# Kernel optimization log

Measured on AMD Instinct MI355X. Metric: run time of the kernel, lower is better.

## Reference

```python
import jax, jax.numpy as jnp
import numpy as np

N_NODES = 50000
N_EDGES = 800000
D_FEAT = 64
THETA = [0.5, 0.3, 0.15, 0.05]  # polynomial filter coefficients, k = len(THETA)


def setup_inputs() -> dict:
    key = jax.random.key(0)
    k1, k2, k3 = jax.random.split(key, 3)
    feat = jax.random.normal(k1, (N_NODES, D_FEAT), dtype=jnp.float32)
    src = jax.random.randint(k2, (N_EDGES,), 0, N_NODES)  # A[src, dst] = 1
    dst = jax.random.randint(k3, (N_EDGES,), 0, N_NODES)
    return {"feat": feat, "src": src, "dst": dst}


def reference(feat, src, dst):
    # normalize_adj: D^{-1/2} A^T D^{-1/2} with D = rowsum(A) (inf -> 0 for isolated nodes).
    n = feat.shape[0]
    deg = jax.ops.segment_sum(jnp.ones(src.shape, dtype=feat.dtype), src, num_segments=n)
    d_inv_sqrt = jnp.where(deg > 0, jax.lax.rsqrt(jnp.maximum(deg, 1.0)), jnp.zeros_like(deg))
    # norm[i, j] = d_i^{-1/2} A[j, i] d_j^{-1/2}; edge (src=j, dst=i) carries weight
    w = d_inv_sqrt[src] * d_inv_sqrt[dst]  # [E]

    def spmm(x):
        # (A_norm @ x)[i] = sum over edges with dst==i of w_e * x[src_e]
        return jax.ops.segment_sum(w[:, None] * x[src], dst, num_segments=n)

    # Original loop: h = theta[0]*(A@f); for k>=1: f = A@f; h += theta[k]*f.
    # Note theta[0] and theta[1] both scale A@f0 (feat is not updated before h init),
    # so we fold them together and avoid recomputing the first SpMM.
    x = spmm(feat)  # A @ f0, shared by the k=0 and k=1 terms
    h = (THETA[0] + THETA[1]) * x
    for k in range(2, len(THETA)):
        x = spmm(x)
        h = h + THETA[k] * x
    return h
```

## Files before the change

kernel.cpp:

```cpp
#include <hip/hip_runtime.h>
#include <hip/hip_bf16.h>

#define N_NODES 50000
#define N_EDGES 800000
#define D_FEAT  64
#define NW      12500
#define G_SRC   64
#define G_DST   256
#define CONV_NB 128
#define FILL_NB 64
#define HB      512
#define SCAN_B  256
#define SCAN_NBLK ((NW + SCAN_B - 1) / SCAN_B)
#define CAP     48


typedef unsigned uint4_ev  __attribute__((ext_vector_type(4)));
typedef float    float4_ev __attribute__((ext_vector_type(4)));

__device__ __forceinline__ float bflo(unsigned u) { return __uint_as_float(u << 16); }
__device__ __forceinline__ float bfhi(unsigned u) { return __uint_as_float(u & 0xFFFF0000u); }
__device__ __forceinline__ unsigned pack_bf16(float a, float b) {
    __hip_bfloat16 x = __float2bfloat16(a), y = __float2bfloat16(b);
    unsigned short ux = *reinterpret_cast<unsigned short*>(&x);
    unsigned short uy = *reinterpret_cast<unsigned short*>(&y);
    return (unsigned)ux | ((unsigned)uy << 16);
}


__global__ void hist_cv_kernel(const int* __restrict__ src, const int* __restrict__ dst,
                               unsigned* __restrict__ psrc_p, unsigned* __restrict__ pdst_p,
                               const float* __restrict__ feat, unsigned* __restrict__ featbf,
                               unsigned* __restrict__ csr, int nE) {
    int t = threadIdx.x;
    int b = blockIdx.x;
    if (b >= G_SRC + G_DST + CONV_NB) {
        int fb = b - (G_SRC + G_DST + CONV_NB);
        uint4* c4 = (uint4*)csr;
        const int n4 = N_NODES * CAP / 4;
        const int nthr = FILL_NB * HB;
        uint4 z = make_uint4(0u, 0u, 0u, 0u);
        for (int i = fb * HB + t; i < n4; i += nthr) c4[i] = z;
        return;
    }
    if (b >= G_SRC + G_DST) {
        int cb = b - (G_SRC + G_DST);
        const float4* f4 = (const float4*)feat;
        uint2* fb2 = (uint2*)featbf;
        const int nthr = CONV_NB * HB;
        for (int i = cb * HB + t; i < N_NODES * 16; i += nthr) {
            float4 v = f4[i];
            fb2[i] = make_uint2(pack_bf16(v.x, v.y), pack_bf16(v.z, v.w));
        }
        return;
    }
    __shared__ unsigned bins[NW];
    for (int i = t; i < NW; i += HB) bins[i] = 0;
    __syncthreads();
    bool is_src = (b < G_SRC);
    int g = is_src ? b : (b - G_SRC);
    int nstr = is_src ? G_SRC : G_DST;
    const int4* k4 = (const int4*)(is_src ? src : dst);
    int nE4 = nE >> 2;
    for (int q = g * HB + t; q < nE4; q += nstr * HB) {
        int4 kv = k4[q];
        atomicAdd(&bins[kv.x >> 2], 1u << (8 * (kv.x & 3)));
        atomicAdd(&bins[kv.y >> 2], 1u << (8 * (kv.y & 3)));
        atomicAdd(&bins[kv.z >> 2], 1u << (8 * (kv.z & 3)));
        atomicAdd(&bins[kv.w >> 2], 1u << (8 * (kv.w & 3)));
    }
    __syncthreads();
    unsigned* p = (is_src ? psrc_p : pdst_p) + g * NW;
    for (int i = t; i < NW; i += HB) p[i] = bins[i];
}

__global__ void scanA_kernel(const unsigned* __restrict__ pdst_p, const unsigned* __restrict__ psrc_p,
                             unsigned* __restrict__ gbase_p, unsigned* __restrict__ deg_p,
                             float* __restrict__ dinv) {
    int w = blockIdx.x * SCAN_B + threadIdx.x;
    if (w >= NW) return;
    unsigned td = 0;
    #pragma unroll 16
    for (int g = 0; g < G_DST; g++) {
        gbase_p[g * NW + w] = td;
        td += pdst_p[g * NW + w];
    }
    deg_p[w] = td;
    unsigned ts = 0;
    #pragma unroll 16
    for (int g = 0; g < G_SRC; g++) ts += psrc_p[g * NW + w];
    unsigned d0 = ts & 255u, d1 = (ts >> 8) & 255u, d2 = (ts >> 16) & 255u, d3 = ts >> 24;
    float4 dv;
    dv.x = d0 ? rsqrtf((float)d0) : 0.0f;
    dv.y = d1 ? rsqrtf((float)d1) : 0.0f;
    dv.z = d2 ? rsqrtf((float)d2) : 0.0f;
    dv.w = d3 ? rsqrtf((float)d3) : 0.0f;
    ((float4*)dinv)[w] = dv;
}

__global__ void scatter_kernel(const int* __restrict__ src, const int* __restrict__ dst,
                               const unsigned* __restrict__ gbase_p, const float* __restrict__ dinv,
                               unsigned* __restrict__ csr, int nE) {
    __shared__ unsigned cur[NW];
    int t = threadIdx.x;
    int g = blockIdx.x;
    const unsigned* gb = gbase_p + (size_t)g * NW;
    for (int i = t; i < NW; i += HB) cur[i] = gb[i];
    __syncthreads();
    const int4* s4 = (const int4*)src;
    const int4* d4 = (const int4*)dst;
    int nE4 = nE >> 2;
    for (int q = g * HB + t; q < nE4; q += G_DST * HB) {
        int4 sv = s4[q];
        int4 dv = d4[q];
        {
            int k = dv.x; int sh = 8 * (k & 3);
            unsigned old = atomicAdd(&cur[k >> 2], 1u << sh);
            unsigned pw = __float2uint_rn(dinv[sv.x] * 32767.0f);
            csr[(size_t)k * CAP + ((old >> sh) & 255u)] = (pw << 17) | (unsigned)sv.x;
        }
        {
            int k = dv.y; int sh = 8 * (k & 3);
            unsigned old = atomicAdd(&cur[k >> 2], 1u << sh);
            unsigned pw = __float2uint_rn(dinv[sv.y] * 32767.0f);
            csr[(size_t)k * CAP + ((old >> sh) & 255u)] = (pw << 17) | (unsigned)sv.y;
        }
        {
            int k = dv.z; int sh = 8 * (k & 3);
            unsigned old = atomicAdd(&cur[k >> 2], 1u << sh);
            unsigned pw = __float2uint_rn(dinv[sv.z] * 32767.0f);
            csr[(size_t)k * CAP + ((old >> sh) & 255u)] = (pw << 17) | (unsigned)sv.z;
        }
        {
            int k = dv.w; int sh = 8 * (k & 3);
            unsigned old = atomicAdd(&cur[k >> 2], 1u << sh);
            unsigned pw = __float2uint_rn(dinv[sv.w] * 32767.0f);
            csr[(size_t)k * CAP + ((old >> sh) & 255u)] = (pw << 17) | (unsigned)sv.w;
        }
    }
}


__device__ __forceinline__ unsigned get_deg(const unsigned* __restrict__ deg_p, int i) {
    return (deg_p[(unsigned)i >> 2] >> (8 * (i & 3))) & 255u;
}

struct Acc8 { float a0, a1, a2, a3, a4, a5, a6, a7; };

__device__ __forceinline__ Acc8 spmm_accum(int ii, int mdr, const unsigned* __restrict__ csr,
                                           const unsigned* __restrict__ x, int c8) {
    const unsigned* row = csr + (size_t)ii * CAP;
    const uint4* x4 = (const uint4*)x;
    const float WS = 1.0f / 32767.0f;
    float a0 = 0, a1 = 0, a2 = 0, a3 = 0, a4 = 0, a5 = 0, a6 = 0, a7 = 0;
    for (int s = 0; s < mdr; s += 4) {
        unsigned v0 = __builtin_nontemporal_load(row + s);
        unsigned v1 = __builtin_nontemporal_load(row + s + 1);
        unsigned v2 = __builtin_nontemporal_load(row + s + 2);
        unsigned v3 = __builtin_nontemporal_load(row + s + 3);
        int   s0 = (int)(v0 & 0x1FFFFu); float w0 = (float)(v0 >> 17) * WS;
        int   s1 = (int)(v1 & 0x1FFFFu); float w1 = (float)(v1 >> 17) * WS;
        int   s2 = (int)(v2 & 0x1FFFFu); float w2 = (float)(v2 >> 17) * WS;
        int   s3 = (int)(v3 & 0x1FFFFu); float w3 = (float)(v3 >> 17) * WS;
        uint4 r0 = x4[(size_t)s0 * 8 + c8];
        uint4 r1 = x4[(size_t)s1 * 8 + c8];
        uint4 r2 = x4[(size_t)s2 * 8 + c8];
        uint4 r3 = x4[(size_t)s3 * 8 + c8];
        a0 += w0 * bflo(r0.x) + w1 * bflo(r1.x) + w2 * bflo(r2.x) + w3 * bflo(r3.x);
        a1 += w0 * bfhi(r0.x) + w1 * bfhi(r1.x) + w2 * bfhi(r2.x) + w3 * bfhi(r3.x);
        a2 += w0 * bflo(r0.y) + w1 * bflo(r1.y) + w2 * bflo(r2.y) + w3 * bflo(r3.y);
        a3 += w0 * bfhi(r0.y) + w1 * bfhi(r1.y) + w2 * bfhi(r2.y) + w3 * bfhi(r3.y);
        a4 += w0 * bflo(r0.z) + w1 * bflo(r1.z) + w2 * bflo(r2.z) + w3 * bflo(r3.z);
        a5 += w0 * bfhi(r0.z) + w1 * bfhi(r1.z) + w2 * bfhi(r2.z) + w3 * bfhi(r3.z);
        a6 += w0 * bflo(r0.w) + w1 * bflo(r1.w) + w2 * bflo(r2.w) + w3 * bflo(r3.w);
        a7 += w0 * bfhi(r0.w) + w1 * bfhi(r1.w) + w2 * bfhi(r2.w) + w3 * bfhi(r3.w);
    }
    Acc8 r = {a0, a1, a2, a3, a4, a5, a6, a7};
    return r;
}

__global__ void spmm_mid_kernel(const unsigned* __restrict__ csr, const unsigned* __restrict__ deg_p,
                                const float* __restrict__ dinv,
                                const unsigned* __restrict__ x, unsigned* __restrict__ y) {
    int tid = blockIdx.x * blockDim.x + threadIdx.x;
    int lane = threadIdx.x & 63;
    int g = lane >> 3, c8 = lane & 7;
    int i = (tid >> 6) * 8 + g;
    bool valid = i < N_NODES;
    int ii = valid ? i : 0;
    int md = valid ? (int)get_deg(deg_p, ii) : 0;
    md = max(md, __shfl_xor(md, 8));
    md = max(md, __shfl_xor(md, 16));
    md = max(md, __shfl_xor(md, 32));
    int mdr = (md + 3) & ~3;
    Acc8 A = spmm_accum(ii, mdr, csr, x, c8);
    if (valid) {
        float di = dinv[i];
        uint4_ev p;
        p.x = pack_bf16(A.a0 * di, A.a1 * di);
        p.y = pack_bf16(A.a2 * di, A.a3 * di);
        p.z = pack_bf16(A.a4 * di, A.a5 * di);
        p.w = pack_bf16(A.a6 * di, A.a7 * di);
        __builtin_nontemporal_store(p, (uint4_ev*)y + (size_t)i * 8 + c8);
    }
}

__global__ void spmm_final_kernel(const unsigned* __restrict__ csr, const unsigned* __restrict__ deg_p,
                                  const float* __restrict__ dinv,
                                  const unsigned* __restrict__ x1, const unsigned* __restrict__ x2,
                                  float* __restrict__ h) {
    int tid = blockIdx.x * blockDim.x + threadIdx.x;
    int lane = threadIdx.x & 63;
    int g = lane >> 3, c8 = lane & 7;
    int i = (tid >> 6) * 8 + g;
    bool valid = i < N_NODES;
    int ii = valid ? i : 0;
    int md = valid ? (int)get_deg(deg_p, ii) : 0;
    md = max(md, __shfl_xor(md, 8));
    md = max(md, __shfl_xor(md, 16));
    md = max(md, __shfl_xor(md, 32));
    int mdr = (md + 3) & ~3;
    Acc8 A = spmm_accum(ii, mdr, csr, x2, c8);
    if (valid) {
        float di = dinv[i] * 0.05f;
        uint4 u1 = ((const uint4*)x1)[(size_t)i * 8 + c8];
        uint4 u2 = ((const uint4*)x2)[(size_t)i * 8 + c8];
        float4_ev o0, o1;
        o0.x = 0.8f * bflo(u1.x) + 0.15f * bflo(u2.x) + di * A.a0;
        o0.y = 0.8f * bfhi(u1.x) + 0.15f * bfhi(u2.x) + di * A.a1;
        o0.z = 0.8f * bflo(u1.y) + 0.15f * bflo(u2.y) + di * A.a2;
        o0.w = 0.8f * bfhi(u1.y) + 0.15f * bfhi(u2.y) + di * A.a3;
        o1.x = 0.8f * bflo(u1.z) + 0.15f * bflo(u2.z) + di * A.a4;
        o1.y = 0.8f * bfhi(u1.z) + 0.15f * bfhi(u2.z) + di * A.a5;
        o1.z = 0.8f * bflo(u1.w) + 0.15f * bflo(u2.w) + di * A.a6;
        o1.w = 0.8f * bfhi(u1.w) + 0.15f * bfhi(u2.w) + di * A.a7;
        float* hp = h + (size_t)i * 64 + c8 * 8;
        __builtin_nontemporal_store(o0, (float4_ev*)hp);
        __builtin_nontemporal_store(o1, (float4_ev*)(hp + 4));
    }
}


extern "C" void kernel_launch(void* const* d_in, const int* in_sizes, int n_in,
                              void* d_out, int out_size, void* d_ws, size_t ws_size,
                              hipStream_t stream) {
    const float* feat = (const float*)d_in[0];
    const int*   src  = (const int*)d_in[1];
    const int*   dst  = (const int*)d_in[2];
    float* h = (float*)d_out;

    char* ws = (char*)d_ws;
    unsigned* psrc_p   = (unsigned*)(ws);
    unsigned* pdst_p   = (unsigned*)(ws +  3200000u);
    unsigned* gbase_p  = (unsigned*)(ws + 16000000u);
    float*    dinv     = (float*)   (ws + 28800000u);
    unsigned* csr      = (unsigned*)(ws + 29000192u);
    unsigned* featbf   = (unsigned*)(ws + 38600192u);
    unsigned* bufA     = (unsigned*)(ws + 45000192u);
    unsigned* bufB     = (unsigned*)(ws + 51400192u);
    unsigned* deg_p    = (unsigned*)(ws + 57800192u);

    const int nE = N_EDGES;
    const int B = 256;

    hist_cv_kernel<<<G_SRC + G_DST + CONV_NB + FILL_NB, HB, 0, stream>>>(
        src, dst, psrc_p, pdst_p, feat, featbf, csr, nE);

    scanA_kernel<<<SCAN_NBLK, SCAN_B, 0, stream>>>(pdst_p, psrc_p, gbase_p, deg_p, dinv);

    scatter_kernel<<<G_DST, HB, 0, stream>>>(src, dst, gbase_p, dinv, csr, nE);

    const int spmmGrid = (N_NODES * 8 + B - 1) / B;
    spmm_mid_kernel<<<spmmGrid, B, 0, stream>>>(csr, deg_p, dinv, featbf, bufA);
    spmm_mid_kernel<<<spmmGrid, B, 0, stream>>>(csr, deg_p, dinv, bufA, bufB);
    spmm_final_kernel<<<spmmGrid, B, 0, stream>>>(csr, deg_p, dinv, bufA, bufB, h);
}
```

Measured before the change: 159.2 us.

## Fold degree normalization into features and shrink CSR to 16-bit indices

Rescales the propagated vectors by D^{-1/2} so the SpMM becomes an unweighted gather-sum. The per-edge weights can then be dropped, and CSR entries shrink from packed 32-bit index+weight to 16-bit indices. Padding slots point to a zero sentinel row, which removes the weight decode and multiply. Feature conversion now happens in the scatter kernel, scaled by dinv, and the final kernel rescales with sqrt(deg). Node indices must fit in 16 bits (50000 does), and storing the rescaled values in bf16 may change rounding error.

Result: faster. 150.2 us (-5.6%).

```diff
diff --git a/kernel.cpp b/kernel.cpp
--- a/kernel.cpp
+++ b/kernel.cpp
@@ -3,19 +3,17 @@
 
 #define N_NODES 50000
 #define N_EDGES 800000
-#define D_FEAT  64
 #define NW      12500
 #define G_SRC   64
 #define G_DST   256
-#define CONV_NB 128
-#define FILL_NB 64
+#define PRE_NB  64
 #define HB      512
-#define SCAN_B  256
-#define SCAN_NBLK ((NW + SCAN_B - 1) / SCAN_B)
+#define SCAN_B  512
+#define SCAN_NBLK 25
 #define CAP     48
-
-
-typedef unsigned uint4_ev  __attribute__((ext_vector_type(4)));
+#define ZROW    50000
+
+
 typedef float    float4_ev __attribute__((ext_vector_type(4)));
 
 __device__ __forceinline__ float bflo(unsigned u) { return __uint_as_float(u << 16); }
@@ -27,30 +25,28 @@
     return (unsigned)ux | ((unsigned)uy << 16);
 }
 
-
-__global__ void hist_cv_kernel(const int* __restrict__ src, const int* __restrict__ dst,
-                               unsigned* __restrict__ psrc_p, unsigned* __restrict__ pdst_p,
-                               const float* __restrict__ feat, unsigned* __restrict__ featbf,
-                               unsigned* __restrict__ csr, int nE) {
+__device__ __forceinline__ unsigned get_deg(const unsigned* __restrict__ deg_p, int i) {
+    return (deg_p[(unsigned)i >> 2] >> (8 * (i & 3))) & 255u;
+}
+
+__global__ void build1_kernel(const int* __restrict__ src, const int* __restrict__ dst,
+                              unsigned* __restrict__ psrc_p, unsigned* __restrict__ pdst_p,
+                              unsigned short* __restrict__ csr16,
+                              unsigned* __restrict__ z0, unsigned* __restrict__ z1,
+                              unsigned* __restrict__ z2, int nE) {
     int t = threadIdx.x;
     int b = blockIdx.x;
-    if (b >= G_SRC + G_DST + CONV_NB) {
-        int fb = b - (G_SRC + G_DST + CONV_NB);
-        uint4* c4 = (uint4*)csr;
-        const int n4 = N_NODES * CAP / 4;
-        const int nthr = FILL_NB * HB;
-        uint4 z = make_uint4(0u, 0u, 0u, 0u);
-        for (int i = fb * HB + t; i < n4; i += nthr) c4[i] = z;
-        return;
-    }
+    int nE4 = nE >> 2;
     if (b >= G_SRC + G_DST) {
-        int cb = b - (G_SRC + G_DST);
-        const float4* f4 = (const float4*)feat;
-        uint2* fb2 = (uint2*)featbf;
-        const int nthr = CONV_NB * HB;
-        for (int i = cb * HB + t; i < N_NODES * 16; i += nthr) {
-            float4 v = f4[i];
-            fb2[i] = make_uint2(pack_bf16(v.x, v.y), pack_bf16(v.z, v.w));
+        int fb = b - (G_SRC + G_DST);
+        uint4* c4 = (uint4*)csr16;
+        const int n4 = N_NODES * CAP / 8;
+        const unsigned SEN2 = ((unsigned)ZROW << 16) | (unsigned)ZROW;
+        uint4 zz = make_uint4(SEN2, SEN2, SEN2, SEN2);
+        for (int i = fb * HB + t; i < n4; i += PRE_NB * HB) c4[i] = zz;
+        if (fb == 0 && t < 96) {
+            unsigned* zp = (t < 32) ? z0 : (t < 64) ? z1 : z2;
+            zp[(size_t)ZROW * 32 + (t & 31)] = 0u;
         }
         return;
     }
@@ -61,7 +57,6 @@
     int g = is_src ? b : (b - G_SRC);
     int nstr = is_src ? G_SRC : G_DST;
     const int4* k4 = (const int4*)(is_src ? src : dst);
-    int nE4 = nE >> 2;
     for (int q = g * HB + t; q < nE4; q += nstr * HB) {
         int4 kv = k4[q];
         atomicAdd(&bins[kv.x >> 2], 1u << (8 * (kv.x & 3)));
@@ -70,170 +65,164 @@
         atomicAdd(&bins[kv.w >> 2], 1u << (8 * (kv.w & 3)));
     }
     __syncthreads();
-    unsigned* p = (is_src ? psrc_p : pdst_p) + g * NW;
+    unsigned* p = (is_src ? psrc_p : pdst_p) + (size_t)g * NW;
     for (int i = t; i < NW; i += HB) p[i] = bins[i];
 }
 
-__global__ void scanA_kernel(const unsigned* __restrict__ pdst_p, const unsigned* __restrict__ psrc_p,
-                             unsigned* __restrict__ gbase_p, unsigned* __restrict__ deg_p,
-                             float* __restrict__ dinv) {
+__global__ void scan_kernel(const unsigned* __restrict__ pdst_p, const unsigned* __restrict__ psrc_p,
+                            unsigned* __restrict__ gbase_p, unsigned* __restrict__ deg_p,
+                            float* __restrict__ dinv, float* __restrict__ sd) {
     int w = blockIdx.x * SCAN_B + threadIdx.x;
     if (w >= NW) return;
     unsigned td = 0;
     #pragma unroll 16
     for (int g = 0; g < G_DST; g++) {
-        gbase_p[g * NW + w] = td;
-        td += pdst_p[g * NW + w];
+        gbase_p[(size_t)g * NW + w] = td;
+        td += pdst_p[(size_t)g * NW + w];
     }
     deg_p[w] = td;
     unsigned ts = 0;
     #pragma unroll 16
-    for (int g = 0; g < G_SRC; g++) ts += psrc_p[g * NW + w];
+    for (int g = 0; g < G_SRC; g++) ts += psrc_p[(size_t)g * NW + w];
     unsigned d0 = ts & 255u, d1 = (ts >> 8) & 255u, d2 = (ts >> 16) & 255u, d3 = ts >> 24;
-    float4 dv;
-    dv.x = d0 ? rsqrtf((float)d0) : 0.0f;
-    dv.y = d1 ? rsqrtf((float)d1) : 0.0f;
-    dv.z = d2 ? rsqrtf((float)d2) : 0.0f;
-    dv.w = d3 ? rsqrtf((float)d3) : 0.0f;
+    float4 dv, sv;
+    dv.x = d0 ? rsqrtf((float)d0) : 0.0f;  sv.x = d0 ? sqrtf((float)d0) : 0.0f;
+    dv.y = d1 ? rsqrtf((float)d1) : 0.0f;  sv.y = d1 ? sqrtf((float)d1) : 0.0f;
+    dv.z = d2 ? rsqrtf((float)d2) : 0.0f;  sv.z = d2 ? sqrtf((float)d2) : 0.0f;
+    dv.w = d3 ? rsqrtf((float)d3) : 0.0f;  sv.w = d3 ? sqrtf((float)d3) : 0.0f;
     ((float4*)dinv)[w] = dv;
-}
-
-__global__ void scatter_kernel(const int* __restrict__ src, const int* __restrict__ dst,
-                               const unsigned* __restrict__ gbase_p, const float* __restrict__ dinv,
-                               unsigned* __restrict__ csr, int nE) {
-    __shared__ unsigned cur[NW];
+    ((float4*)sd)[w] = sv;
+}
+
+__global__ void scatter_conv_kernel(const int* __restrict__ src, const int* __restrict__ dst,
+                                    const unsigned* __restrict__ gbase_p,
+                                    const float* __restrict__ feat, const float* __restrict__ dinv,
+                                    unsigned short* __restrict__ csr16, unsigned* __restrict__ z0,
+                                    int nE) {
     int t = threadIdx.x;
-    int g = blockIdx.x;
-    const unsigned* gb = gbase_p + (size_t)g * NW;
-    for (int i = t; i < NW; i += HB) cur[i] = gb[i];
-    __syncthreads();
-    const int4* s4 = (const int4*)src;
-    const int4* d4 = (const int4*)dst;
+    int b = blockIdx.x;
     int nE4 = nE >> 2;
-    for (int q = g * HB + t; q < nE4; q += G_DST * HB) {
-        int4 sv = s4[q];
-        int4 dv = d4[q];
-        {
-            int k = dv.x; int sh = 8 * (k & 3);
-            unsigned old = atomicAdd(&cur[k >> 2], 1u << sh);
-            unsigned pw = __float2uint_rn(dinv[sv.x] * 32767.0f);
-            csr[(size_t)k * CAP + ((old >> sh) & 255u)] = (pw << 17) | (unsigned)sv.x;
+    if (b < G_DST) {
+        __shared__ unsigned cur[NW];
+        const unsigned* gb = gbase_p + (size_t)b * NW;
+        for (int i = t; i < NW; i += HB) cur[i] = gb[i];
+        __syncthreads();
+        const int4* s4 = (const int4*)src;
+        const int4* d4 = (const int4*)dst;
+        for (int q = b * HB + t; q < nE4; q += G_DST * HB) {
+            int4 sv = s4[q];
+            int4 dv = d4[q];
+            { int k = dv.x; int sh = 8 * (k & 3);
+              unsigned old = atomicAdd(&cur[k >> 2], 1u << sh);
+              csr16[(size_t)k * CAP + ((old >> sh) & 255u)] = (unsigned short)sv.x; }
+            { int k = dv.y; int sh = 8 * (k & 3);
+              unsigned old = atomicAdd(&cur[k >> 2], 1u << sh);
+              csr16[(size_t)k * CAP + ((old >> sh) & 255u)] = (unsigned short)sv.y; }
+            { int k = dv.z; int sh = 8 * (k & 3);
+              unsigned old = atomicAdd(&cur[k >> 2], 1u << sh);
+              csr16[(size_t)k * CAP + ((old >> sh) & 255u)] = (unsigned short)sv.z; }
+            { int k = dv.w; int sh = 8 * (k & 3);
+              unsigned old = atomicAdd(&cur[k >> 2], 1u << sh);
+              csr16[(size_t)k * CAP + ((old >> sh) & 255u)] = (unsigned short)sv.w; }
         }
-        {
-            int k = dv.y; int sh = 8 * (k & 3);
-            unsigned old = atomicAdd(&cur[k >> 2], 1u << sh);
-            unsigned pw = __float2uint_rn(dinv[sv.y] * 32767.0f);
-            csr[(size_t)k * CAP + ((old >> sh) & 255u)] = (pw << 17) | (unsigned)sv.y;
+    } else {
+        const float4* f4 = (const float4*)feat;
+        for (int i = (b - G_DST) * HB + t; i < N_NODES * 16; i += (512 - G_DST) * HB) {
+            float4 v = f4[i];
+            int node = i >> 4, off = i & 15;
+            float dv = dinv[node];
+            ((uint2*)z0)[(size_t)node * 16 + off] =
+                make_uint2(pack_bf16(v.x * dv, v.y * dv), pack_bf16(v.z * dv, v.w * dv));
         }
-        {
-            int k = dv.z; int sh = 8 * (k & 3);
-            unsigned old = atomicAdd(&cur[k >> 2], 1u << sh);
-            unsigned pw = __float2uint_rn(dinv[sv.z] * 32767.0f);
-            csr[(size_t)k * CAP + ((old >> sh) & 255u)] = (pw << 17) | (unsigned)sv.z;
-        }
-        {
-            int k = dv.w; int sh = 8 * (k & 3);
-            unsigned old = atomicAdd(&cur[k >> 2], 1u << sh);
-            unsigned pw = __float2uint_rn(dinv[sv.w] * 32767.0f);
-            csr[(size_t)k * CAP + ((old >> sh) & 255u)] = (pw << 17) | (unsigned)sv.w;
-        }
-    }
-}
-
-
-__device__ __forceinline__ unsigned get_deg(const unsigned* __restrict__ deg_p, int i) {
-    return (deg_p[(unsigned)i >> 2] >> (8 * (i & 3))) & 255u;
+    }
 }
 
 struct Acc8 { float a0, a1, a2, a3, a4, a5, a6, a7; };
 
-__device__ __forceinline__ Acc8 spmm_accum(int ii, int mdr, const unsigned* __restrict__ csr,
-                                           const unsigned* __restrict__ x, int c8) {
-    const unsigned* row = csr + (size_t)ii * CAP;
-    const uint4* x4 = (const uint4*)x;
-    const float WS = 1.0f / 32767.0f;
+__device__ __forceinline__ Acc8 gather_slots(const unsigned short* __restrict__ csr16,
+                                             const unsigned* __restrict__ zin,
+                                             int ii, int mdr, int c8) {
+    const unsigned short* row = csr16 + (size_t)ii * CAP;
+    const uint4* x4 = (const uint4*)zin;
     float a0 = 0, a1 = 0, a2 = 0, a3 = 0, a4 = 0, a5 = 0, a6 = 0, a7 = 0;
     for (int s = 0; s < mdr; s += 4) {
-        unsigned v0 = __builtin_nontemporal_load(row + s);
-        unsigned v1 = __builtin_nontemporal_load(row + s + 1);
-        unsigned v2 = __builtin_nontemporal_load(row + s + 2);
-        unsigned v3 = __builtin_nontemporal_load(row + s + 3);
-        int   s0 = (int)(v0 & 0x1FFFFu); float w0 = (float)(v0 >> 17) * WS;
-        int   s1 = (int)(v1 & 0x1FFFFu); float w1 = (float)(v1 >> 17) * WS;
-        int   s2 = (int)(v2 & 0x1FFFFu); float w2 = (float)(v2 >> 17) * WS;
-        int   s3 = (int)(v3 & 0x1FFFFu); float w3 = (float)(v3 >> 17) * WS;
+        uint2 vv = *(const uint2*)(row + s);
+        int s0 = (int)(vv.x & 0xFFFFu), s1 = (int)(vv.x >> 16);
+        int s2 = (int)(vv.y & 0xFFFFu), s3 = (int)(vv.y >> 16);
         uint4 r0 = x4[(size_t)s0 * 8 + c8];
         uint4 r1 = x4[(size_t)s1 * 8 + c8];
         uint4 r2 = x4[(size_t)s2 * 8 + c8];
         uint4 r3 = x4[(size_t)s3 * 8 + c8];
-        a0 += w0 * bflo(r0.x) + w1 * bflo(r1.x) + w2 * bflo(r2.x) + w3 * bflo(r3.x);
-        a1 += w0 * bfhi(r0.x) + w1 * bfhi(r1.x) + w2 * bfhi(r2.x) + w3 * bfhi(r3.x);
-        a2 += w0 * bflo(r0.y) + w1 * bflo(r1.y) + w2 * bflo(r2.y) + w3 * bflo(r3.y);
-        a3 += w0 * bfhi(r0.y) + w1 * bfhi(r1.y) + w2 * bfhi(r2.y) + w3 * bfhi(r3.y);
-        a4 += w0 * bflo(r0.z) + w1 * bflo(r1.z) + w2 * bflo(r2.z) + w3 * bflo(r3.z);
-        a5 += w0 * bfhi(r0.z) + w1 * bfhi(r1.z) + w2 * bfhi(r2.z) + w3 * bfhi(r3.z);
-        a6 += w0 * bflo(r0.w) + w1 * bflo(r1.w) + w2 * bflo(r2.w) + w3 * bflo(r3.w);
-        a7 += w0 * bfhi(r0.w) + w1 * bfhi(r1.w) + w2 * bfhi(r2.w) + w3 * bfhi(r3.w);
+        a0 += (bflo(r0.x) + bflo(r1.x)) + (bflo(r2.x) + bflo(r3.x));
+        a1 += (bfhi(r0.x) + bfhi(r1.x)) + (bfhi(r2.x) + bfhi(r3.x));
+        a2 += (bflo(r0.y) + bflo(r1.y)) + (bflo(r2.y) + bflo(r3.y));
+        a3 += (bfhi(r0.y) + bfhi(r1.y)) + (bfhi(r2.y) + bfhi(r3.y));
+        a4 += (bflo(r0.z) + bflo(r1.z)) + (bflo(r2.z) + bflo(r3.z));
+        a5 += (bfhi(r0.z) + bfhi(r1.z)) + (bfhi(r2.z) + bfhi(r3.z));
+        a6 += (bflo(r0.w) + bflo(r1.w)) + (bflo(r2.w) + bflo(r3.w));
+        a7 += (bfhi(r0.w) + bfhi(r1.w)) + (bfhi(r2.w) + bfhi(r3.w));
     }
     Acc8 r = {a0, a1, a2, a3, a4, a5, a6, a7};
     return r;
 }
 
-__global__ void spmm_mid_kernel(const unsigned* __restrict__ csr, const unsigned* __restrict__ deg_p,
-                                const float* __restrict__ dinv,
-                                const unsigned* __restrict__ x, unsigned* __restrict__ y) {
+__global__ void spmm_mid_kernel(const unsigned short* __restrict__ csr16,
+                                const unsigned* __restrict__ deg_p, const float* __restrict__ dinv,
+                                const unsigned* __restrict__ zin, unsigned* __restrict__ zout) {
     int tid = blockIdx.x * blockDim.x + threadIdx.x;
     int lane = threadIdx.x & 63;
-    int g = lane >> 3, c8 = lane & 7;
-    int i = (tid >> 6) * 8 + g;
+    int gg = lane >> 3, c8 = lane & 7;
+    int i = (tid >> 6) * 8 + gg;
     bool valid = i < N_NODES;
     int ii = valid ? i : 0;
     int md = valid ? (int)get_deg(deg_p, ii) : 0;
     md = max(md, __shfl_xor(md, 8));
     md = max(md, __shfl_xor(md, 16));
     md = max(md, __shfl_xor(md, 32));
-    int mdr = (md + 3) & ~3;
-    Acc8 A = spmm_accum(ii, mdr, csr, x, c8);
+    int mdr = min((md + 3) & ~3, CAP);
+    Acc8 A = gather_slots(csr16, zin, ii, mdr, c8);
     if (valid) {
-        float di = dinv[i];
-        uint4_ev p;
-        p.x = pack_bf16(A.a0 * di, A.a1 * di);
-        p.y = pack_bf16(A.a2 * di, A.a3 * di);
-        p.z = pack_bf16(A.a4 * di, A.a5 * di);
-        p.w = pack_bf16(A.a6 * di, A.a7 * di);
-        __builtin_nontemporal_store(p, (uint4_ev*)y + (size_t)i * 8 + c8);
-    }
-}
-
-__global__ void spmm_final_kernel(const unsigned* __restrict__ csr, const unsigned* __restrict__ deg_p,
-                                  const float* __restrict__ dinv,
-                                  const unsigned* __restrict__ x1, const unsigned* __restrict__ x2,
+        float di = dinv[i], di2 = di * di;
+        uint4 p;
+        p.x = pack_bf16(A.a0 * di2, A.a1 * di2);
+        p.y = pack_bf16(A.a2 * di2, A.a3 * di2);
+        p.z = pack_bf16(A.a4 * di2, A.a5 * di2);
+        p.w = pack_bf16(A.a6 * di2, A.a7 * di2);
+        ((uint4*)zout)[(size_t)i * 8 + c8] = p;
+    }
+}
+
+__global__ void spmm_final_kernel(const unsigned short* __restrict__ csr16,
+                                  const unsigned* __restrict__ deg_p, const float* __restrict__ dinv,
+                                  const float* __restrict__ sd,
+                                  const unsigned* __restrict__ z1, const unsigned* __restrict__ z2,
                                   float* __restrict__ h) {
     int tid = blockIdx.x * blockDim.x + threadIdx.x;
     int lane = threadIdx.x & 63;
-    int g = lane >> 3, c8 = lane & 7;
-    int i = (tid >> 6) * 8 + g;
+    int gg = lane >> 3, c8 = lane & 7;
+    int i = (tid >> 6) * 8 + gg;
     bool valid = i < N_NODES;
     int ii = valid ? i : 0;
     int md = valid ? (int)get_deg(deg_p, ii) : 0;
     md = max(md, __shfl_xor(md, 8));
     md = max(md, __shfl_xor(md, 16));
     md = max(md, __shfl_xor(md, 32));
-    int mdr = (md + 3) & ~3;
-    Acc8 A = spmm_accum(ii, mdr, csr, x2, c8);
+    int mdr = min((md + 3) & ~3, CAP);
+    Acc8 A = gather_slots(csr16, z2, ii, mdr, c8);
     if (valid) {
-        float di = dinv[i] * 0.05f;
-        uint4 u1 = ((const uint4*)x1)[(size_t)i * 8 + c8];
-        uint4 u2 = ((const uint4*)x2)[(size_t)i * 8 + c8];
+        float s_ = sd[i];
+        float c1 = 0.8f * s_, c2 = 0.15f * s_, c3 = 0.05f * dinv[i];
+        uint4 u1 = ((const uint4*)z1)[(size_t)i * 8 + c8];
+        uint4 u2 = ((const uint4*)z2)[(size_t)i * 8 + c8];
         float4_ev o0, o1;
-        o0.x = 0.8f * bflo(u1.x) + 0.15f * bflo(u2.x) + di * A.a0;
-        o0.y = 0.8f * bfhi(u1.x) + 0.15f * bfhi(u2.x) + di * A.a1;
-        o0.z = 0.8f * bflo(u1.y) + 0.15f * bflo(u2.y) + di * A.a2;
-        o0.w = 0.8f * bfhi(u1.y) + 0.15f * bfhi(u2.y) + di * A.a3;
-        o1.x = 0.8f * bflo(u1.z) + 0.15f * bflo(u2.z) + di * A.a4;
-        o1.y = 0.8f * bfhi(u1.z) + 0.15f * bfhi(u2.z) + di * A.a5;
-        o1.z = 0.8f * bflo(u1.w) + 0.15f * bflo(u2.w) + di * A.a6;
-        o1.w = 0.8f * bfhi(u1.w) + 0.15f * bfhi(u2.w) + di * A.a7;
+        o0.x = c1 * bflo(u1.x) + c2 * bflo(u2.x) + c3 * A.a0;
+        o0.y = c1 * bfhi(u1.x) + c2 * bfhi(u2.x) + c3 * A.a1;
+        o0.z = c1 * bflo(u1.y) + c2 * bflo(u2.y) + c3 * A.a2;
+        o0.w = c1 * bfhi(u1.y) + c2 * bfhi(u2.y) + c3 * A.a3;
+        o1.x = c1 * bflo(u1.z) + c2 * bflo(u2.z) + c3 * A.a4;
+        o1.y = c1 * bfhi(u1.z) + c2 * bfhi(u2.z) + c3 * A.a5;
+        o1.z = c1 * bflo(u1.w) + c2 * bflo(u2.w) + c3 * A.a6;
+        o1.w = c1 * bfhi(u1.w) + c2 * bfhi(u2.w) + c3 * A.a7;
         float* hp = h + (size_t)i * 64 + c8 * 8;
         __builtin_nontemporal_store(o0, (float4_ev*)hp);
         __builtin_nontemporal_store(o1, (float4_ev*)(hp + 4));
@@ -250,28 +239,29 @@
     float* h = (float*)d_out;
 
     char* ws = (char*)d_ws;
-    unsigned* psrc_p   = (unsigned*)(ws);
-    unsigned* pdst_p   = (unsigned*)(ws +  3200000u);
-    unsigned* gbase_p  = (unsigned*)(ws + 16000000u);
-    float*    dinv     = (float*)   (ws + 28800000u);
-    unsigned* csr      = (unsigned*)(ws + 29000192u);
-    unsigned* featbf   = (unsigned*)(ws + 38600192u);
-    unsigned* bufA     = (unsigned*)(ws + 45000192u);
-    unsigned* bufB     = (unsigned*)(ws + 51400192u);
-    unsigned* deg_p    = (unsigned*)(ws + 57800192u);
+    unsigned*       psrc_p  = (unsigned*)      (ws);
+    unsigned*       pdst_p  = (unsigned*)      (ws +  3200000u);
+    unsigned*       gbase_p = (unsigned*)      (ws + 16000000u);
+    unsigned*       deg_p   = (unsigned*)      (ws + 28800000u);
+    float*          dinv    = (float*)         (ws + 28850176u);
+    float*          sd      = (float*)         (ws + 29050368u);
+    unsigned short* csr16   = (unsigned short*)(ws + 29250560u);
+    unsigned*       z0      = (unsigned*)      (ws + 34050560u);
+    unsigned*       z1      = (unsigned*)      (ws + 40452608u);
+    unsigned*       z2      = (unsigned*)      (ws + 46854656u);
 
     const int nE = N_EDGES;
+
+    build1_kernel<<<G_SRC + G_DST + PRE_NB, HB, 0, stream>>>(
+        src, dst, psrc_p, pdst_p, csr16, z0, z1, z2, nE);
+
+    scan_kernel<<<SCAN_NBLK, SCAN_B, 0, stream>>>(pdst_p, psrc_p, gbase_p, deg_p, dinv, sd);
+
+    scatter_conv_kernel<<<512, HB, 0, stream>>>(src, dst, gbase_p, feat, dinv, csr16, z0, nE);
+
     const int B = 256;
-
-    hist_cv_kernel<<<G_SRC + G_DST + CONV_NB + FILL_NB, HB, 0, stream>>>(
-        src, dst, psrc_p, pdst_p, feat, featbf, csr, nE);
-
-    scanA_kernel<<<SCAN_NBLK, SCAN_B, 0, stream>>>(pdst_p, psrc_p, gbase_p, deg_p, dinv);
-
-    scatter_kernel<<<G_DST, HB, 0, stream>>>(src, dst, gbase_p, dinv, csr, nE);
-
     const int spmmGrid = (N_NODES * 8 + B - 1) / B;
-    spmm_mid_kernel<<<spmmGrid, B, 0, stream>>>(csr, deg_p, dinv, featbf, bufA);
-    spmm_mid_kernel<<<spmmGrid, B, 0, stream>>>(csr, deg_p, dinv, bufA, bufB);
-    spmm_final_kernel<<<spmmGrid, B, 0, stream>>>(csr, deg_p, dinv, bufA, bufB, h);
-}
+    spmm_mid_kernel<<<spmmGrid, B, 0, stream>>>(csr16, deg_p, dinv, z0, z1);
+    spmm_mid_kernel<<<spmmGrid, B, 0, stream>>>(csr16, deg_p, dinv, z1, z2);
+    spmm_final_kernel<<<spmmGrid, B, 0, stream>>>(csr16, deg_p, dinv, sd, z1, z2, h);
+}
```
